# Optimization experiments

Hardware: AMD Instinct MI355X
Metric: run time of the kernel (lower is better)

The kernel has to match this reference:

```python
import jax, jax.numpy as jnp
import numpy as np

B, S, D_IN, D_OUT, H = 4, 2048, 1024, 1024, 16
HD = D_OUT // H


def setup_inputs() -> dict:
    key = jax.random.key(0)
    ks = jax.random.split(key, 6)
    s_in = 1.0 / np.sqrt(D_IN)
    s_out = 1.0 / np.sqrt(D_OUT)
    return {
        "x": jax.random.normal(ks[0], (B, S, D_IN), dtype=jnp.float32),
        "W_q": jax.random.uniform(ks[1], (D_OUT, D_IN), jnp.float32, -s_in, s_in),
        "W_k": jax.random.uniform(ks[2], (D_OUT, D_IN), jnp.float32, -s_in, s_in),
        "W_v": jax.random.uniform(ks[3], (D_OUT, D_IN), jnp.float32, -s_in, s_in),
        "W_o": jax.random.uniform(ks[4], (D_OUT, D_OUT), jnp.float32, -s_out, s_out),
        "b_o": jax.random.uniform(ks[5], (D_OUT,), jnp.float32, -s_out, s_out),
    }


def reference(x, W_q, W_k, W_v, W_o, b_o):
    b, s, _ = x.shape
    # torch Linear: y = x @ W.T  (no qkv bias)
    q = (x @ W_q.T).reshape(b, s, H, HD).transpose(0, 2, 1, 3)  # [b,h,s,hd]
    k = (x @ W_k.T).reshape(b, s, H, HD).transpose(0, 2, 1, 3)
    v = (x @ W_v.T).reshape(b, s, H, HD).transpose(0, 2, 1, 3)
    scores = jnp.einsum("bhqd,bhkd->bhqk", q, k)  # [b,h,s,s]
    causal = jnp.triu(jnp.ones((s, s), dtype=bool), k=1)
    scores = jnp.where(causal, -jnp.inf, scores)
    attn = jax.nn.softmax(scores / np.sqrt(HD), axis=-1)
    # dropout p=0.0 -> identity
    ctx = jnp.einsum("bhqk,bhkd->bhqd", attn, v)  # [b,h,s,hd]
    ctx = ctx.transpose(0, 2, 1, 3).reshape(b, s, D_OUT)
    return ctx @ W_o.T + b_o
```

## Files before the change

### kernel.cpp

```cpp
#include <hip/hip_runtime.h>
#include <cstdint>
#include <cstddef>

#define S_LEN  2048
#define NHEAD  16
#define HDIM   64
#define KD     1024
#define BSROWS 8192

typedef __attribute__((ext_vector_type(4))) float          floatx4;
typedef __attribute__((ext_vector_type(8))) __bf16         bf16x8;
typedef __attribute__((ext_vector_type(8))) unsigned short ushort8v;
typedef __attribute__((ext_vector_type(4))) unsigned short ushort4v;
typedef __attribute__((ext_vector_type(4))) float          float4v;

__device__ __forceinline__ unsigned short f2bf(float f) {
  unsigned int u = __float_as_uint(f);
  u += 0x7fffu + ((u >> 16) & 1u);
  return (unsigned short)(u >> 16);
}

#if __has_builtin(__builtin_amdgcn_exp2f)
#define EXP2F(x) __builtin_amdgcn_exp2f(x)
#else
#define EXP2F(x) exp2f(x)
#endif

__device__ __forceinline__ unsigned int pack2bf(float a, float b) {
#if __has_builtin(__builtin_amdgcn_perm)
  return __builtin_amdgcn_perm(__float_as_uint(b), __float_as_uint(a), 0x07060302);
#else
  return (__float_as_uint(a) >> 16) | (__float_as_uint(b) & 0xffff0000u);
#endif
}

__device__ __forceinline__ void async_cp16(const void* gsrc, void* ldst) {
  __builtin_amdgcn_global_load_lds(
      (__attribute__((address_space(1))) void*)gsrc,
      (__attribute__((address_space(3))) void*)ldst,
      16, 0, 0);
}

#define XN4 2097152
#define WN4 262144

__global__ __launch_bounds__(256) void cvt_kernel(
    const float* __restrict__ x,  const float* __restrict__ wq,
    const float* __restrict__ wk, const float* __restrict__ wv,
    const float* __restrict__ wo,
    unsigned short* __restrict__ xb, unsigned short* __restrict__ wqkvb,
    unsigned short* __restrict__ wob)
{
  const int i = blockIdx.x * 256 + threadIdx.x;
  const float* src; unsigned short* dst; int off;
  if (i < XN4) { src = x; dst = xb; off = i; }
  else {
    const int j = i - XN4;
    if (j < WN4)          { src = wq; dst = wqkvb;           off = j; }
    else if (j < 2*WN4)   { src = wk; dst = wqkvb + 4*WN4;   off = j - WN4; }
    else if (j < 3*WN4)   { src = wv; dst = wqkvb + 8*WN4;   off = j - 2*WN4; }
    else                  { src = wo; dst = wob;             off = j - 3*WN4; }
  }
  const float4v v = ((const float4v*)src)[off];
  ushort4v o;
  o.x = f2bf(v.x); o.y = f2bf(v.y); o.z = f2bf(v.z); o.w = f2bf(v.w);
  ((ushort4v*)dst)[off] = o;
}

__global__ __launch_bounds__(256) void gemm_qkv(
    const unsigned short* __restrict__ A,
    const unsigned short* __restrict__ Bw,
    unsigned short* __restrict__ Qo,
    unsigned short* __restrict__ Ko,
    unsigned short* __restrict__ Vto)
{
  __shared__ unsigned short smem[17408];
  const int tid  = threadIdx.x;
  const int wave = tid >> 6, lane = tid & 63;
  const int quad = lane >> 4, l15 = lane & 15;
  const int wr = wave >> 1, wc = wave & 1;
  const int m0 = blockIdx.x * 128, n0 = blockIdx.y * 128;

  const int srow = lane >> 2;
  const int scol = ((lane & 3) ^ ((srow >> 1) & 3)) * 8;
  const unsigned short* gA = A  + (size_t)(m0 + wave * 32 + srow) * KD + scol;
  const unsigned short* gB = Bw + (size_t)(n0 + wave * 32 + srow) * KD + scol;

  const floatx4 fzero = {0.f, 0.f, 0.f, 0.f};
  floatx4 acc[4][4];
#pragma unroll
  for (int i = 0; i < 4; i++)
#pragma unroll
    for (int j = 0; j < 4; j++) acc[i][j] = fzero;

  {
    unsigned short* lA = smem + wave * 1024;
    unsigned short* lB = smem + 4096 + wave * 1024;
    async_cp16(gA,                    lA);
    async_cp16(gA + (size_t)16 * KD,  lA + 512);
    async_cp16(gB,                    lB);
    async_cp16(gB + (size_t)16 * KD,  lB + 512);
  }
  const int lsw = (l15 >> 1) & 3;

#pragma unroll 2
  for (int it = 0; it < 32; it++) {
    asm volatile("s_waitcnt vmcnt(0) lgkmcnt(0)\n\ts_barrier" ::: "memory");
    if (it + 1 < 32) {
      const int nb = (it + 1) & 1;
      const int ko = (it + 1) * 32;
      unsigned short* lA = smem + nb * 8192 + wave * 1024;
      unsigned short* lB = smem + nb * 8192 + 4096 + wave * 1024;
      async_cp16(gA + ko,                   lA);
      async_cp16(gA + ko + (size_t)16 * KD, lA + 512);
      async_cp16(gB + ko,                   lB);
      async_cp16(gB + ko + (size_t)16 * KD, lB + 512);
    }
    const unsigned short* As = smem + (it & 1) * 8192;
    const unsigned short* Bs = As + 4096;

    bf16x8 af[4], bfrag[4];
#pragma unroll
    for (int i = 0; i < 4; i++)
      af[i] = *(const bf16x8*)&As[(wr * 64 + i * 16 + l15) * 32 + (quad ^ lsw) * 8];
#pragma unroll
    for (int j = 0; j < 4; j++)
      bfrag[j] = *(const bf16x8*)&Bs[(wc * 64 + j * 16 + l15) * 32 + (quad ^ lsw) * 8];
#pragma unroll
    for (int i = 0; i < 4; i++)
#pragma unroll
      for (int j = 0; j < 4; j++)
        acc[i][j] = __builtin_amdgcn_mfma_f32_16x16x32_bf16(af[i], bfrag[j], acc[i][j], 0, 0, 0);
  }

  const int which = n0 >> 10;
  const int h0 = (n0 & 1023) >> 6;
  const int b = m0 >> 11, sl = m0 & 2047;

  if (which < 2) {
    unsigned short* dst = which ? Ko : Qo;
    const float scale = which ? 1.0f : 0.18033688011112042f;
    __syncthreads();
    const int crow = wr * 64 + quad * 4;
    const int ccol = wc * 64 + l15;
#pragma unroll
    for (int i = 0; i < 4; i++)
#pragma unroll
      for (int j = 0; j < 4; j++)
#pragma unroll
        for (int r = 0; r < 4; r++)
          smem[(crow + i * 16 + r) * 130 + ccol + j * 16] = f2bf(acc[i][j][r] * scale);
    __syncthreads();
#pragma unroll
    for (int t = 0; t < 8; t++) {
      const int c   = t * 256 + tid;
      const int hd8 = (c & 7) * 8;
      const int hh  = (c >> 3) & 1;
      const int s   = c >> 4;
      const ushort8v val = *(const ushort8v*)&smem[s * 130 + hh * 64 + hd8];
      *(ushort8v*)&dst[((size_t)((b * NHEAD + h0 + hh) * S_LEN + sl + s)) * HDIM + hd8] = val;
    }
  } else {
    __syncthreads();
    const int crow = wr * 64 + quad * 4;
    const int ccol = wc * 64 + l15;
#pragma unroll
    for (int i = 0; i < 4; i++)
#pragma unroll
      for (int j = 0; j < 4; j++) {
        ushort4v t4;
#pragma unroll
        for (int r = 0; r < 4; r++) t4[r] = f2bf(acc[i][j][r]);
        *(ushort4v*)&smem[(ccol + j * 16) * 136 + crow + i * 16] = t4;
      }
    __syncthreads();
#pragma unroll
    for (int t = 0; t < 8; t++) {
      const int c  = t * 256 + tid;
      const int nl = c >> 4, sc = (c & 15) * 8;
      const ushort8v val = *(const ushort8v*)&smem[nl * 136 + sc];
      *(ushort8v*)&Vto[((size_t)((b * NHEAD + h0 + (nl >> 6)) * HDIM + (nl & 63))) * S_LEN + sl + sc] = val;
    }
  }
}

__global__ __launch_bounds__(512, 6) void attn_kernel(
    const unsigned short* __restrict__ Qg_,
    const unsigned short* __restrict__ Kg_,
    const unsigned short* __restrict__ Vtg_,
    unsigned short* __restrict__ CTX)
{
  __shared__ unsigned short smem[25088];
  const int tid  = threadIdx.x, wave = tid >> 6, lane = tid & 63;
  const int quad = lane >> 4, l15 = lane & 15;
  unsigned short* Pw = smem + 16384 + wave * 1088;

  const int bh = (int)blockIdx.x;
  const int yy = (int)blockIdx.y;
  const int qt = (yy < 4) ? yy : (yy < 8) ? (11 - yy) : (yy < 12) ? yy : (27 - yy);
  const int q0 = qt * 128;
  const size_t base = (size_t)bh * (S_LEN * HDIM);
  const unsigned short* Qg  = Qg_  + base;
  const unsigned short* Kg  = Kg_  + base;
  const unsigned short* Vtg = Vtg_ + base;
  const int qw = q0 + wave * 16;

  const int strow = lane >> 3;
  const int stxc  = (lane & 7) ^ strow;
  const unsigned short* kstage = Kg  + (size_t)(wave * 8 + strow) * HDIM  + stxc * 8;
  const unsigned short* vstage = Vtg + (size_t)(wave * 8 + strow) * S_LEN + stxc * 8;
  unsigned short* kd0 = smem + wave * 512;
  unsigned short* vd0 = smem + 4096 + wave * 512;

  async_cp16(kstage, kd0);
  async_cp16(vstage, vd0);

  bf16x8 qf[2];
#pragma unroll
  for (int ks = 0; ks < 2; ks++)
    qf[ks] = *(const bf16x8*)&Qg[(size_t)(qw + l15) * HDIM + ks * 32 + quad * 8];

  const int sw0 = ((quad)     ^ (l15 & 7)) * 8;
  const int sw1 = ((4 + quad) ^ (l15 & 7)) * 8;

  const floatx4 fzero = {0.f, 0.f, 0.f, 0.f};
  floatx4 O[4];
  float l_part = 0.f;
#pragma unroll
  for (int mt = 0; mt < 4; mt++) O[mt] = fzero;

  const int ntiles = 2 * qt + 2;

  for (int j = 0; j < ntiles; j++) {
    asm volatile("s_waitcnt vmcnt(0) lgkmcnt(0)\n\ts_barrier" ::: "memory");
    if (j + 1 < ntiles) {
      const int nb = (j + 1) & 1;
      async_cp16(kstage + (size_t)(j + 1) * 64 * HDIM, kd0 + nb * 8192);
      async_cp16(vstage + (size_t)(j + 1) * 64,        vd0 + nb * 8192);
    }
    const int k0 = j * 64;
    if (k0 > qw + 15) continue;
    const unsigned short* Ksb = smem + (j & 1) * 8192;
    const unsigned short* Vsb = Ksb + 4096;
    const int krel = qw + 15 - k0;

    floatx4 sa[4];
#pragma unroll
    for (int kt = 0; kt < 4; kt++) sa[kt] = fzero;
    __builtin_amdgcn_s_setprio(1);
#pragma unroll
    for (int kt = 0; kt < 4; kt++) {
      if (kt * 16 <= krel) {
        const unsigned short* kr = &Ksb[(kt * 16 + l15) * 64];
        sa[kt] = __builtin_amdgcn_mfma_f32_16x16x32_bf16(*(const bf16x8*)(kr + sw0), qf[0], sa[kt], 0, 0, 0);
        sa[kt] = __builtin_amdgcn_mfma_f32_16x16x32_bf16(*(const bf16x8*)(kr + sw1), qf[1], sa[kt], 0, 0, 0);
      }
    }
    __builtin_amdgcn_s_setprio(0);

    const int qrow = qw + l15;
#pragma unroll
    for (int kt = 0; kt < 4; kt++) {
      const int kbase = k0 + kt * 16;
      unsigned short* pdst = &Pw[l15 * 68 + kt * 16 + quad * 4];
      if (kt * 16 <= krel) {
        if (kbase + 15 > qw) {
#pragma unroll
          for (int r = 0; r < 4; r++)
            if (kbase + quad * 4 + r > qrow) sa[kt][r] = -INFINITY;
        }
        const float p0 = EXP2F(sa[kt][0]), p1 = EXP2F(sa[kt][1]);
        const float p2 = EXP2F(sa[kt][2]), p3 = EXP2F(sa[kt][3]);
        l_part += (p0 + p1) + (p2 + p3);
        uint2 pk; pk.x = pack2bf(p0, p1); pk.y = pack2bf(p2, p3);
        *(uint2*)pdst = pk;
      } else if ((kt >> 1) * 32 <= krel) {
        uint2 z; z.x = 0u; z.y = 0u;
        *(uint2*)pdst = z;
      }
    }
    asm volatile("s_waitcnt lgkmcnt(0)" ::: "memory");

#pragma unroll
    for (int ks = 0; ks < 2; ks++) {
      if (ks * 32 > krel) break;
      const unsigned short* ps = &Pw[l15 * 68 + ks * 32 + quad * 8];
      union { ushort4v h[2]; bf16x8 v; } pu;
      pu.h[0] = *(const ushort4v*)ps;
      pu.h[1] = *(const ushort4v*)(ps + 4);
      __builtin_amdgcn_s_setprio(1);
#pragma unroll
      for (int mt = 0; mt < 4; mt++) {
        const bf16x8 vf = *(const bf16x8*)(&Vsb[(mt * 16 + l15) * 64] + (ks ? sw1 : sw0));
        O[mt] = __builtin_amdgcn_mfma_f32_16x16x32_bf16(vf, pu.v, O[mt], 0, 0, 0);
      }
      __builtin_amdgcn_s_setprio(0);
    }
  }

#pragma unroll
  for (int d = 16; d < 64; d <<= 1)
    l_part += __shfl_xor(l_part, d, 64);

  {
    const float inv = 1.0f / l_part;
#pragma unroll
    for (int mt = 0; mt < 4; mt++)
#pragma unroll
      for (int a = 0; a < 2; a++) {
        const unsigned int pk =
            (unsigned int)f2bf(O[mt][2 * a] * inv) |
            ((unsigned int)f2bf(O[mt][2 * a + 1] * inv) << 16);
        *(unsigned int*)&Pw[l15 * 68 + mt * 16 + quad * 4 + 2 * a] = pk;
      }
  }
  asm volatile("s_waitcnt lgkmcnt(0)" ::: "memory");
  const int b = bh >> 4, h = bh & 15;
#pragma unroll
  for (int it = 0; it < 2; it++) {
    const int g = it * 64 + lane;
    const int row = g >> 3, c8 = (g & 7) * 8;
    union { ushort4v h[2]; ushort8v v; } ou;
    ou.h[0] = *(const ushort4v*)&Pw[row * 68 + c8];
    ou.h[1] = *(const ushort4v*)&Pw[row * 68 + c8 + 4];
    const int s = qw + row;
    *(ushort8v*)&CTX[((size_t)(b * S_LEN + s)) * KD + h * HDIM + c8] = ou.v;
  }
}

__global__ __launch_bounds__(256) void gemm_out(
    const unsigned short* __restrict__ A,
    const unsigned short* __restrict__ Bw,
    const float* __restrict__ bias,
    float* __restrict__ out)
{
  __shared__ unsigned short smem[16384];
  const int tid  = threadIdx.x;
  const int wave = tid >> 6, lane = tid & 63;
  const int quad = lane >> 4, l15 = lane & 15;
  const int wr = wave >> 1, wc = wave & 1;
  const int m0 = blockIdx.x * 128, n0 = blockIdx.y * 128;

  const int srow = lane >> 2;
  const int scol = ((lane & 3) ^ ((srow >> 1) & 3)) * 8;
  const unsigned short* gA = A  + (size_t)(m0 + wave * 32 + srow) * KD + scol;
  const unsigned short* gB = Bw + (size_t)(n0 + wave * 32 + srow) * KD + scol;

  const floatx4 fzero = {0.f, 0.f, 0.f, 0.f};
  floatx4 acc[4][4];
#pragma unroll
  for (int i = 0; i < 4; i++)
#pragma unroll
    for (int j = 0; j < 4; j++) acc[i][j] = fzero;

  {
    unsigned short* lA = smem + wave * 1024;
    unsigned short* lB = smem + 4096 + wave * 1024;
    async_cp16(gA,                    lA);
    async_cp16(gA + (size_t)16 * KD,  lA + 512);
    async_cp16(gB,                    lB);
    async_cp16(gB + (size_t)16 * KD,  lB + 512);
  }
  const int lsw = (l15 >> 1) & 3;

#pragma unroll 2
  for (int it = 0; it < 32; it++) {
    asm volatile("s_waitcnt vmcnt(0) lgkmcnt(0)\n\ts_barrier" ::: "memory");
    if (it + 1 < 32) {
      const int nb = (it + 1) & 1;
      const int ko = (it + 1) * 32;
      unsigned short* lA = smem + nb * 8192 + wave * 1024;
      unsigned short* lB = smem + nb * 8192 + 4096 + wave * 1024;
      async_cp16(gA + ko,                   lA);
      async_cp16(gA + ko + (size_t)16 * KD, lA + 512);
      async_cp16(gB + ko,                   lB);
      async_cp16(gB + ko + (size_t)16 * KD, lB + 512);
    }
    const unsigned short* As = smem + (it & 1) * 8192;
    const unsigned short* Bs = As + 4096;

    bf16x8 af[4], bfrag[4];
#pragma unroll
    for (int i = 0; i < 4; i++)
      af[i] = *(const bf16x8*)&As[(wr * 64 + i * 16 + l15) * 32 + (quad ^ lsw) * 8];
#pragma unroll
    for (int j = 0; j < 4; j++)
      bfrag[j] = *(const bf16x8*)&Bs[(wc * 64 + j * 16 + l15) * 32 + (quad ^ lsw) * 8];
#pragma unroll
    for (int i = 0; i < 4; i++)
#pragma unroll
      for (int j = 0; j < 4; j++)
        acc[i][j] = __builtin_amdgcn_mfma_f32_16x16x32_bf16(af[i], bfrag[j], acc[i][j], 0, 0, 0);
  }

#pragma unroll
  for (int j = 0; j < 4; j++) {
    const int n = n0 + wc * 64 + j * 16 + l15;
    const float bb = bias[n];
#pragma unroll
    for (int i = 0; i < 4; i++) {
#pragma unroll
      for (int r = 0; r < 4; r++) {
        const int m = m0 + wr * 64 + i * 16 + quad * 4 + r;
        out[(size_t)m * KD + n] = acc[i][j][r] + bb;
      }
    }
  }
}

extern "C" void kernel_launch(void* const* d_in, const int* in_sizes, int n_in,
                              void* d_out, int out_size, void* d_ws, size_t ws_size,
                              hipStream_t stream) {
  (void)in_sizes; (void)n_in; (void)out_size;
  const float* x  = (const float*)d_in[0];
  const float* wq = (const float*)d_in[1];
  const float* wk = (const float*)d_in[2];
  const float* wv = (const float*)d_in[3];
  const float* wo = (const float*)d_in[4];
  const float* bo = (const float*)d_in[5];
  float* out = (float*)d_out;

  if (ws_size < (size_t)92274688) return;
  char* ws = (char*)d_ws;
  unsigned short* xb    = (unsigned short*)(ws);
  unsigned short* wqkvb = (unsigned short*)(ws + (size_t)16777216);
  unsigned short* wob   = (unsigned short*)(ws + (size_t)23068672);
  unsigned short* qws   = (unsigned short*)(ws + (size_t)25165824);
  unsigned short* kws   = (unsigned short*)(ws + (size_t)41943040);
  unsigned short* vtws  = (unsigned short*)(ws + (size_t)58720256);
  unsigned short* ctxws = (unsigned short*)(ws + (size_t)75497472);

  cvt_kernel<<<12288, 256, 0, stream>>>(x, wq, wk, wv, wo, xb, wqkvb, wob);
  gemm_qkv<<<dim3(64, 24), 256, 0, stream>>>(xb, wqkvb, qws, kws, vtws);
  attn_kernel<<<dim3(64, 16), 512, 0, stream>>>(qws, kws, vtws, ctxws);
  gemm_out<<<dim3(64, 8), 256, 0, stream>>>(ctxws, wob, bo, out);
}
```

Before: 239.2 us.

## Load GEMM weight fragments straight from global into registers, swap MFMA operands

In the QKV and output GEMMs, the B (weight) tile is no longer staged through LDS. Each wave loads its B fragments directly from global memory into registers with a one-iteration register prefetch. This halves LDS use and cuts LDS traffic, at the cost of uncoalesced-ish global loads and more register pressure. For the Q/K and output paths the MFMA operands are swapped so the result is transposed, which allows vectorized ushort4 LDS writes and float4 output/bias stores. The QKV launch is split into a Q/K kernel and a V kernel through a template.

```diff
diff --git a/kernel.cpp b/kernel.cpp
--- a/kernel.cpp
+++ b/kernel.cpp
@@ -67,7 +67,8 @@
   ((ushort4v*)dst)[off] = o;
 }
 
-__global__ __launch_bounds__(256) void gemm_qkv(
+template<bool ISV>
+__global__ __launch_bounds__(256) void gemm_qkv_t(
     const unsigned short* __restrict__ A,
     const unsigned short* __restrict__ Bw,
     unsigned short* __restrict__ Qo,
@@ -79,12 +80,14 @@
   const int wave = tid >> 6, lane = tid & 63;
   const int quad = lane >> 4, l15 = lane & 15;
   const int wr = wave >> 1, wc = wave & 1;
-  const int m0 = blockIdx.x * 128, n0 = blockIdx.y * 128;
+  const int m0 = blockIdx.x * 128;
+  const int n0 = ((int)blockIdx.y + (ISV ? 16 : 0)) * 128;
 
   const int srow = lane >> 2;
   const int scol = ((lane & 3) ^ ((srow >> 1) & 3)) * 8;
-  const unsigned short* gA = A  + (size_t)(m0 + wave * 32 + srow) * KD + scol;
-  const unsigned short* gB = Bw + (size_t)(n0 + wave * 32 + srow) * KD + scol;
+  const unsigned short* gA = A + (size_t)(m0 + wave * 32 + srow) * KD + scol;
+
+  const unsigned short* gBf = Bw + (size_t)(n0 + wc * 64 + l15) * KD + quad * 8;
 
   const floatx4 fzero = {0.f, 0.f, 0.f, 0.f};
   floatx4 acc[4][4];
@@ -95,12 +98,14 @@
 
   {
     unsigned short* lA = smem + wave * 1024;
-    unsigned short* lB = smem + 4096 + wave * 1024;
-    async_cp16(gA,                    lA);
-    async_cp16(gA + (size_t)16 * KD,  lA + 512);
-    async_cp16(gB,                    lB);
-    async_cp16(gB + (size_t)16 * KD,  lB + 512);
-  }
+    async_cp16(gA,                   lA);
+    async_cp16(gA + (size_t)16 * KD, lA + 512);
+  }
+  bf16x8 bcur[4], bnext[4];
+#pragma unroll
+  for (int j = 0; j < 4; j++)
+    bcur[j] = *(const bf16x8*)&gBf[(size_t)j * 16 * KD];
+
   const int lsw = (l15 >> 1) & 3;
 
 #pragma unroll 2
@@ -109,47 +114,51 @@
     if (it + 1 < 32) {
       const int nb = (it + 1) & 1;
       const int ko = (it + 1) * 32;
-      unsigned short* lA = smem + nb * 8192 + wave * 1024;
-      unsigned short* lB = smem + nb * 8192 + 4096 + wave * 1024;
+      unsigned short* lA = smem + nb * 4096 + wave * 1024;
       async_cp16(gA + ko,                   lA);
       async_cp16(gA + ko + (size_t)16 * KD, lA + 512);
-      async_cp16(gB + ko,                   lB);
-      async_cp16(gB + ko + (size_t)16 * KD, lB + 512);
-    }
-    const unsigned short* As = smem + (it & 1) * 8192;
-    const unsigned short* Bs = As + 4096;
-
-    bf16x8 af[4], bfrag[4];
+#pragma unroll
+      for (int j = 0; j < 4; j++)
+        bnext[j] = *(const bf16x8*)&gBf[(size_t)j * 16 * KD + ko];
+    }
+    const unsigned short* As = smem + (it & 1) * 4096;
+
+    bf16x8 af[4];
 #pragma unroll
     for (int i = 0; i < 4; i++)
       af[i] = *(const bf16x8*)&As[(wr * 64 + i * 16 + l15) * 32 + (quad ^ lsw) * 8];
 #pragma unroll
-    for (int j = 0; j < 4; j++)
-      bfrag[j] = *(const bf16x8*)&Bs[(wc * 64 + j * 16 + l15) * 32 + (quad ^ lsw) * 8];
-#pragma unroll
-    for (int i = 0; i < 4; i++)
-#pragma unroll
-      for (int j = 0; j < 4; j++)
-        acc[i][j] = __builtin_amdgcn_mfma_f32_16x16x32_bf16(af[i], bfrag[j], acc[i][j], 0, 0, 0);
-  }
-
-  const int which = n0 >> 10;
+    for (int i = 0; i < 4; i++)
+#pragma unroll
+      for (int j = 0; j < 4; j++) {
+        if (ISV)
+          acc[i][j] = __builtin_amdgcn_mfma_f32_16x16x32_bf16(af[i], bcur[j], acc[i][j], 0, 0, 0);
+        else
+          acc[i][j] = __builtin_amdgcn_mfma_f32_16x16x32_bf16(bcur[j], af[i], acc[i][j], 0, 0, 0);
+      }
+#pragma unroll
+    for (int j = 0; j < 4; j++) bcur[j] = bnext[j];
+  }
+
   const int h0 = (n0 & 1023) >> 6;
   const int b = m0 >> 11, sl = m0 & 2047;
 
-  if (which < 2) {
+  if (!ISV) {
+    const int which = n0 >> 10;
     unsigned short* dst = which ? Ko : Qo;
     const float scale = which ? 1.0f : 0.18033688011112042f;
     __syncthreads();
-    const int crow = wr * 64 + quad * 4;
-    const int ccol = wc * 64 + l15;
-#pragma unroll
-    for (int i = 0; i < 4; i++)
-#pragma unroll
-      for (int j = 0; j < 4; j++)
-#pragma unroll
-        for (int r = 0; r < 4; r++)
-          smem[(crow + i * 16 + r) * 130 + ccol + j * 16] = f2bf(acc[i][j][r] * scale);
+    const int srw = wr * 64 + l15;
+    const int scl = wc * 64 + quad * 4;
+#pragma unroll
+    for (int i = 0; i < 4; i++)
+#pragma unroll
+      for (int j = 0; j < 4; j++) {
+        ushort4v t4;
+#pragma unroll
+        for (int r = 0; r < 4; r++) t4[r] = f2bf(acc[i][j][r] * scale);
+        *(ushort4v*)&smem[(srw + i * 16) * 136 + scl + j * 16] = t4;
+      }
     __syncthreads();
 #pragma unroll
     for (int t = 0; t < 8; t++) {
@@ -157,7 +166,7 @@
       const int hd8 = (c & 7) * 8;
       const int hh  = (c >> 3) & 1;
       const int s   = c >> 4;
-      const ushort8v val = *(const ushort8v*)&smem[s * 130 + hh * 64 + hd8];
+      const ushort8v val = *(const ushort8v*)&smem[s * 136 + hh * 64 + hd8];
       *(ushort8v*)&dst[((size_t)((b * NHEAD + h0 + hh) * S_LEN + sl + s)) * HDIM + hd8] = val;
     }
   } else {
@@ -334,7 +343,7 @@
     const float* __restrict__ bias,
     float* __restrict__ out)
 {
-  __shared__ unsigned short smem[16384];
+  __shared__ unsigned short smem[8192];
   const int tid  = threadIdx.x;
   const int wave = tid >> 6, lane = tid & 63;
   const int quad = lane >> 4, l15 = lane & 15;
@@ -343,8 +352,8 @@
 
   const int srow = lane >> 2;
   const int scol = ((lane & 3) ^ ((srow >> 1) & 3)) * 8;
-  const unsigned short* gA = A  + (size_t)(m0 + wave * 32 + srow) * KD + scol;
-  const unsigned short* gB = Bw + (size_t)(n0 + wave * 32 + srow) * KD + scol;
+  const unsigned short* gA = A + (size_t)(m0 + wave * 32 + srow) * KD + scol;
+  const unsigned short* gBf = Bw + (size_t)(n0 + wc * 64 + l15) * KD + quad * 8;
 
   const floatx4 fzero = {0.f, 0.f, 0.f, 0.f};
   floatx4 acc[4][4];
@@ -355,12 +364,14 @@
 
   {
     unsigned short* lA = smem + wave * 1024;
-    unsigned short* lB = smem + 4096 + wave * 1024;
-    async_cp16(gA,                    lA);
-    async_cp16(gA + (size_t)16 * KD,  lA + 512);
-    async_cp16(gB,                    lB);
-    async_cp16(gB + (size_t)16 * KD,  lB + 512);
-  }
+    async_cp16(gA,                   lA);
+    async_cp16(gA + (size_t)16 * KD, lA + 512);
+  }
+  bf16x8 bcur[4], bnext[4];
+#pragma unroll
+  for (int j = 0; j < 4; j++)
+    bcur[j] = *(const bf16x8*)&gBf[(size_t)j * 16 * KD];
+
   const int lsw = (l15 >> 1) & 3;
 
 #pragma unroll 2
@@ -369,41 +380,39 @@
     if (it + 1 < 32) {
       const int nb = (it + 1) & 1;
       const int ko = (it + 1) * 32;
-      unsigned short* lA = smem + nb * 8192 + wave * 1024;
-      unsigned short* lB = smem + nb * 8192 + 4096 + wave * 1024;
+      unsigned short* lA = smem + nb * 4096 + wave * 1024;
       async_cp16(gA + ko,                   lA);
       async_cp16(gA + ko + (size_t)16 * KD, lA + 512);
-      async_cp16(gB + ko,                   lB);
-      async_cp16(gB + ko + (size_t)16 * KD, lB + 512);
-    }
-    const unsigned short* As = smem + (it & 1) * 8192;
-    const unsigned short* Bs = As + 4096;
-
-    bf16x8 af[4], bfrag[4];
+#pragma unroll
+      for (int j = 0; j < 4; j++)
+        bnext[j] = *(const bf16x8*)&gBf[(size_t)j * 16 * KD + ko];
+    }
+    const unsigned short* As = smem + (it & 1) * 4096;
+
+    bf16x8 af[4];
 #pragma unroll
     for (int i = 0; i < 4; i++)
       af[i] = *(const bf16x8*)&As[(wr * 64 + i * 16 + l15) * 32 + (quad ^ lsw) * 8];
 #pragma unroll
-    for (int j = 0; j < 4; j++)
-      bfrag[j] = *(const bf16x8*)&Bs[(wc * 64 + j * 16 + l15) * 32 + (quad ^ lsw) * 8];
-#pragma unroll
     for (int i = 0; i < 4; i++)
 #pragma unroll
       for (int j = 0; j < 4; j++)
-        acc[i][j] = __builtin_amdgcn_mfma_f32_16x16x32_bf16(af[i], bfrag[j], acc[i][j], 0, 0, 0);
+        acc[i][j] = __builtin_amdgcn_mfma_f32_16x16x32_bf16(bcur[j], af[i], acc[i][j], 0, 0, 0);
+#pragma unroll
+    for (int j = 0; j < 4; j++) bcur[j] = bnext[j];
   }
 
 #pragma unroll
   for (int j = 0; j < 4; j++) {
-    const int n = n0 + wc * 64 + j * 16 + l15;
-    const float bb = bias[n];
+    const int nb4 = n0 + wc * 64 + j * 16 + quad * 4;
+    const float4v bb = *(const float4v*)&bias[nb4];
 #pragma unroll
     for (int i = 0; i < 4; i++) {
-#pragma unroll
-      for (int r = 0; r < 4; r++) {
-        const int m = m0 + wr * 64 + i * 16 + quad * 4 + r;
-        out[(size_t)m * KD + n] = acc[i][j][r] + bb;
-      }
+      const int m = m0 + wr * 64 + i * 16 + l15;
+      float4v st;
+#pragma unroll
+      for (int r = 0; r < 4; r++) st[r] = acc[i][j][r] + bb[r];
+      *(float4v*)&out[(size_t)m * KD + nb4] = st;
     }
   }
 }
@@ -431,7 +440,8 @@
   unsigned short* ctxws = (unsigned short*)(ws + (size_t)75497472);
 
   cvt_kernel<<<12288, 256, 0, stream>>>(x, wq, wk, wv, wo, xb, wqkvb, wob);
-  gemm_qkv<<<dim3(64, 24), 256, 0, stream>>>(xb, wqkvb, qws, kws, vtws);
+  gemm_qkv_t<false><<<dim3(64, 16), 256, 0, stream>>>(xb, wqkvb, qws, kws, vtws);
+  gemm_qkv_t<true ><<<dim3(64,  8), 256, 0, stream>>>(xb, wqkvb, qws, kws, vtws);
   attn_kernel<<<dim3(64, 16), 512, 0, stream>>>(qws, kws, vtws, ctxws);
   gemm_out<<<dim3(64, 8), 256, 0, stream>>>(ctxws, wob, bo, out);
 }
```

Result: slower. 306.9 us (+28.3%).
